# Kernel tuning notes

Hardware: AMD Instinct MI355X
Metric: run time of the kernel (lower is better)

The kernel has to match this reference:

```python
import jax, jax.numpy as jnp
import numpy as np

L, B = 64, 7          # n_layers, n_bit_options
EPS = 0.02            # sinkhorn entropic regularizer
ITERS = 200           # sinkhorn iterations
TINY = 1e-40


def setup_inputs() -> dict:
    key = jax.random.key(0)
    k1, k2, k3, k4 = jax.random.split(key, 4)
    theta = jax.random.normal(k1, (L, B), dtype=jnp.float32)
    phi = jax.random.normal(k2, (B,), dtype=jnp.float32)
    # layer sizes (param counts), positive; matches layer_sizes buffer usage
    n = jax.random.uniform(k3, (L,), dtype=jnp.float32, minval=4096.0, maxval=262144.0)
    sens = jax.random.uniform(k4, (L,), dtype=jnp.float32)
    sens = sens / sens.sum()  # update_sensitivity normalizes to a distribution
    bits = jnp.arange(2, 2 + B, dtype=jnp.float32)
    err = 2.0 ** (-2.0 * bits)  # quantization error per bitwidth
    return {"theta": theta, "phi": phi, "n": n, "sens": sens, "err": err}


def reference(theta, phi, n, sens, err):
    # DiffAllocator.compute_P
    a = n / n.sum()                         # row marginal (buffer 'a')
    b = jax.nn.softmax(phi)                 # col marginal b()
    C = (n * sens)[:, None] * err[None, :]  # build_cost: [L,B]
    K = -(C - theta) / EPS                  # log-kernel
    log_a = jnp.log(a + TINY)
    log_b = jnp.log(b + TINY)
    f0 = jnp.zeros((L,), dtype=theta.dtype)
    g0 = jnp.zeros((B,), dtype=theta.dtype)

    def step(carry, _):
        f, g = carry
        f = log_a - jax.scipy.special.logsumexp(K + g[None, :], axis=1)
        g = log_b - jax.scipy.special.logsumexp(K + f[:, None], axis=0)
        return (f, g), None

    (f, g), _ = jax.lax.scan(step, (f0, g0), None, length=ITERS)
    P = jnp.exp(K + f[:, None] + g[None, :])
    return P / (P.sum() + TINY)
```

## Files before the change

kernel.cpp:

```cpp
#include <hip/hip_runtime.h>
#include <math.h>

#define NB 7
#define EPS_ 0.02f
#define ITERS1_ 120
#define ITERS2_ 80
#define TINY_ 1e-40f
#define LOG2E_ 1.4426950408889634f
#define LN2_   0.6931471805599453f

__device__ __forceinline__ float exp2_hw(float x) {
#if __has_builtin(__builtin_amdgcn_exp2f)
    return __builtin_amdgcn_exp2f(x);
#else
    return __expf(x * LN2_);
#endif
}
__device__ __forceinline__ float log2_hw(float x) {
#if __has_builtin(__builtin_amdgcn_logf)
    return __builtin_amdgcn_logf(x);
#else
    return __logf(x) * LOG2E_;
#endif
}
__device__ __forceinline__ float rcp_hw(float x) {
#if __has_builtin(__builtin_amdgcn_rcpf)
    return __builtin_amdgcn_rcpf(x);
#else
    return 1.0f / x;
#endif
}

template <int CTRL>
__device__ __forceinline__ float dpp_ident(float identity, float x) {
    return __int_as_float(__builtin_amdgcn_update_dpp(
        __float_as_int(identity), __float_as_int(x), CTRL, 0xF, 0xF, false));
}
__device__ __forceinline__ float readlane63(float x) {
    return __int_as_float(__builtin_amdgcn_readlane(__float_as_int(x), 63));
}
__device__ __forceinline__ float wave_sum_bcast(float s) {
    s += dpp_ident<0x111>(0.f, s);
    s += dpp_ident<0x112>(0.f, s);
    s += dpp_ident<0x114>(0.f, s);
    s += dpp_ident<0x118>(0.f, s);
    s += dpp_ident<0x142>(0.f, s);
    s += dpp_ident<0x143>(0.f, s);
    return readlane63(s);
}

#define WAVE_MAX7(v0,v1,v2,v3,v4,v5,v6, m0,m1,m2,m3,m4,m5,m6)                 \
  {                                                                           \
    float r0,r1,r2,r3,r4,r5,r6;                                               \
    asm("v_mov_b32 %0, %14\n\t"                                               \
        "v_mov_b32 %1, %15\n\t"                                               \
        "v_mov_b32 %2, %16\n\t"                                               \
        "v_mov_b32 %3, %17\n\t"                                               \
        "v_mov_b32 %4, %18\n\t"                                               \
        "v_mov_b32 %5, %19\n\t"                                               \
        "v_mov_b32 %6, %20\n\t"                                               \
        "v_max_f32_dpp %0, %0, %0 row_shr:1 row_mask:0xf bank_mask:0xf\n\t"   \
        "v_max_f32_dpp %1, %1, %1 row_shr:1 row_mask:0xf bank_mask:0xf\n\t"   \
        "v_max_f32_dpp %2, %2, %2 row_shr:1 row_mask:0xf bank_mask:0xf\n\t"   \
        "v_max_f32_dpp %3, %3, %3 row_shr:1 row_mask:0xf bank_mask:0xf\n\t"   \
        "v_max_f32_dpp %4, %4, %4 row_shr:1 row_mask:0xf bank_mask:0xf\n\t"   \
        "v_max_f32_dpp %5, %5, %5 row_shr:1 row_mask:0xf bank_mask:0xf\n\t"   \
        "v_max_f32_dpp %6, %6, %6 row_shr:1 row_mask:0xf bank_mask:0xf\n\t"   \
        "v_max_f32_dpp %0, %0, %0 row_shr:2 row_mask:0xf bank_mask:0xf\n\t"   \
        "v_max_f32_dpp %1, %1, %1 row_shr:2 row_mask:0xf bank_mask:0xf\n\t"   \
        "v_max_f32_dpp %2, %2, %2 row_shr:2 row_mask:0xf bank_mask:0xf\n\t"   \
        "v_max_f32_dpp %3, %3, %3 row_shr:2 row_mask:0xf bank_mask:0xf\n\t"   \
        "v_max_f32_dpp %4, %4, %4 row_shr:2 row_mask:0xf bank_mask:0xf\n\t"   \
        "v_max_f32_dpp %5, %5, %5 row_shr:2 row_mask:0xf bank_mask:0xf\n\t"   \
        "v_max_f32_dpp %6, %6, %6 row_shr:2 row_mask:0xf bank_mask:0xf\n\t"   \
        "v_max_f32_dpp %0, %0, %0 row_shr:4 row_mask:0xf bank_mask:0xf\n\t"   \
        "v_max_f32_dpp %1, %1, %1 row_shr:4 row_mask:0xf bank_mask:0xf\n\t"   \
        "v_max_f32_dpp %2, %2, %2 row_shr:4 row_mask:0xf bank_mask:0xf\n\t"   \
        "v_max_f32_dpp %3, %3, %3 row_shr:4 row_mask:0xf bank_mask:0xf\n\t"   \
        "v_max_f32_dpp %4, %4, %4 row_shr:4 row_mask:0xf bank_mask:0xf\n\t"   \
        "v_max_f32_dpp %5, %5, %5 row_shr:4 row_mask:0xf bank_mask:0xf\n\t"   \
        "v_max_f32_dpp %6, %6, %6 row_shr:4 row_mask:0xf bank_mask:0xf\n\t"   \
        "v_max_f32_dpp %0, %0, %0 row_shr:8 row_mask:0xf bank_mask:0xf\n\t"   \
        "v_max_f32_dpp %1, %1, %1 row_shr:8 row_mask:0xf bank_mask:0xf\n\t"   \
        "v_max_f32_dpp %2, %2, %2 row_shr:8 row_mask:0xf bank_mask:0xf\n\t"   \
        "v_max_f32_dpp %3, %3, %3 row_shr:8 row_mask:0xf bank_mask:0xf\n\t"   \
        "v_max_f32_dpp %4, %4, %4 row_shr:8 row_mask:0xf bank_mask:0xf\n\t"   \
        "v_max_f32_dpp %5, %5, %5 row_shr:8 row_mask:0xf bank_mask:0xf\n\t"   \
        "v_max_f32_dpp %6, %6, %6 row_shr:8 row_mask:0xf bank_mask:0xf\n\t"   \
        "v_max_f32_dpp %0, %0, %0 row_bcast:15 row_mask:0xa bank_mask:0xf\n\t"\
        "v_max_f32_dpp %1, %1, %1 row_bcast:15 row_mask:0xa bank_mask:0xf\n\t"\
        "v_max_f32_dpp %2, %2, %2 row_bcast:15 row_mask:0xa bank_mask:0xf\n\t"\
        "v_max_f32_dpp %3, %3, %3 row_bcast:15 row_mask:0xa bank_mask:0xf\n\t"\
        "v_max_f32_dpp %4, %4, %4 row_bcast:15 row_mask:0xa bank_mask:0xf\n\t"\
        "v_max_f32_dpp %5, %5, %5 row_bcast:15 row_mask:0xa bank_mask:0xf\n\t"\
        "v_max_f32_dpp %6, %6, %6 row_bcast:15 row_mask:0xa bank_mask:0xf\n\t"\
        "v_max_f32_dpp %0, %0, %0 row_bcast:31 row_mask:0xc bank_mask:0xf\n\t"\
        "v_max_f32_dpp %1, %1, %1 row_bcast:31 row_mask:0xc bank_mask:0xf\n\t"\
        "v_max_f32_dpp %2, %2, %2 row_bcast:31 row_mask:0xc bank_mask:0xf\n\t"\
        "v_max_f32_dpp %3, %3, %3 row_bcast:31 row_mask:0xc bank_mask:0xf\n\t"\
        "v_max_f32_dpp %4, %4, %4 row_bcast:31 row_mask:0xc bank_mask:0xf\n\t"\
        "v_max_f32_dpp %5, %5, %5 row_bcast:31 row_mask:0xc bank_mask:0xf\n\t"\
        "v_max_f32_dpp %6, %6, %6 row_bcast:31 row_mask:0xc bank_mask:0xf\n\t"\
        "v_readlane_b32 %7, %0, 63\n\t"                                       \
        "v_readlane_b32 %8, %1, 63\n\t"                                       \
        "v_readlane_b32 %9, %2, 63\n\t"                                       \
        "v_readlane_b32 %10, %3, 63\n\t"                                      \
        "v_readlane_b32 %11, %4, 63\n\t"                                      \
        "v_readlane_b32 %12, %5, 63\n\t"                                      \
        "v_readlane_b32 %13, %6, 63\n\t"                                      \
        "s_nop 1"                                                             \
        : "=&v"(r0), "=&v"(r1), "=&v"(r2), "=&v"(r3),                         \
          "=&v"(r4), "=&v"(r5), "=&v"(r6),                                    \
          "=s"(m0), "=s"(m1), "=s"(m2), "=s"(m3),                             \
          "=s"(m4), "=s"(m5), "=s"(m6)                                        \
        : "v"(v0), "v"(v1), "v"(v2), "v"(v3), "v"(v4), "v"(v5), "v"(v6));     \
  }

#define WAVE_SUM7(e0,e1,e2,e3,e4,e5,e6, s0_,s1_,s2_,s3_,s4_,s5_,s6_)          \
    asm("s_nop 1\n\t"                                                         \
        "v_add_f32_dpp %0, %0, %0 row_shr:1 row_mask:0xf bank_mask:0xf\n\t"   \
        "v_add_f32_dpp %1, %1, %1 row_shr:1 row_mask:0xf bank_mask:0xf\n\t"   \
        "v_add_f32_dpp %2, %2, %2 row_shr:1 row_mask:0xf bank_mask:0xf\n\t"   \
        "v_add_f32_dpp %3, %3, %3 row_shr:1 row_mask:0xf bank_mask:0xf\n\t"   \
        "v_add_f32_dpp %4, %4, %4 row_shr:1 row_mask:0xf bank_mask:0xf\n\t"   \
        "v_add_f32_dpp %5, %5, %5 row_shr:1 row_mask:0xf bank_mask:0xf\n\t"   \
        "v_add_f32_dpp %6, %6, %6 row_shr:1 row_mask:0xf bank_mask:0xf\n\t"   \
        "v_add_f32_dpp %0, %0, %0 row_shr:2 row_mask:0xf bank_mask:0xf\n\t"   \
        "v_add_f32_dpp %1, %1, %1 row_shr:2 row_mask:0xf bank_mask:0xf\n\t"   \
        "v_add_f32_dpp %2, %2, %2 row_shr:2 row_mask:0xf bank_mask:0xf\n\t"   \
        "v_add_f32_dpp %3, %3, %3 row_shr:2 row_mask:0xf bank_mask:0xf\n\t"   \
        "v_add_f32_dpp %4, %4, %4 row_shr:2 row_mask:0xf bank_mask:0xf\n\t"   \
        "v_add_f32_dpp %5, %5, %5 row_shr:2 row_mask:0xf bank_mask:0xf\n\t"   \
        "v_add_f32_dpp %6, %6, %6 row_shr:2 row_mask:0xf bank_mask:0xf\n\t"   \
        "v_add_f32_dpp %0, %0, %0 row_shr:4 row_mask:0xf bank_mask:0xf\n\t"   \
        "v_add_f32_dpp %1, %1, %1 row_shr:4 row_mask:0xf bank_mask:0xf\n\t"   \
        "v_add_f32_dpp %2, %2, %2 row_shr:4 row_mask:0xf bank_mask:0xf\n\t"   \
        "v_add_f32_dpp %3, %3, %3 row_shr:4 row_mask:0xf bank_mask:0xf\n\t"   \
        "v_add_f32_dpp %4, %4, %4 row_shr:4 row_mask:0xf bank_mask:0xf\n\t"   \
        "v_add_f32_dpp %5, %5, %5 row_shr:4 row_mask:0xf bank_mask:0xf\n\t"   \
        "v_add_f32_dpp %6, %6, %6 row_shr:4 row_mask:0xf bank_mask:0xf\n\t"   \
        "v_add_f32_dpp %0, %0, %0 row_shr:8 row_mask:0xf bank_mask:0xf\n\t"   \
        "v_add_f32_dpp %1, %1, %1 row_shr:8 row_mask:0xf bank_mask:0xf\n\t"   \
        "v_add_f32_dpp %2, %2, %2 row_shr:8 row_mask:0xf bank_mask:0xf\n\t"   \
        "v_add_f32_dpp %3, %3, %3 row_shr:8 row_mask:0xf bank_mask:0xf\n\t"   \
        "v_add_f32_dpp %4, %4, %4 row_shr:8 row_mask:0xf bank_mask:0xf\n\t"   \
        "v_add_f32_dpp %5, %5, %5 row_shr:8 row_mask:0xf bank_mask:0xf\n\t"   \
        "v_add_f32_dpp %6, %6, %6 row_shr:8 row_mask:0xf bank_mask:0xf\n\t"   \
        "v_add_f32_dpp %0, %0, %0 row_bcast:15 row_mask:0xa bank_mask:0xf\n\t"\
        "v_add_f32_dpp %1, %1, %1 row_bcast:15 row_mask:0xa bank_mask:0xf\n\t"\
        "v_add_f32_dpp %2, %2, %2 row_bcast:15 row_mask:0xa bank_mask:0xf\n\t"\
        "v_add_f32_dpp %3, %3, %3 row_bcast:15 row_mask:0xa bank_mask:0xf\n\t"\
        "v_add_f32_dpp %4, %4, %4 row_bcast:15 row_mask:0xa bank_mask:0xf\n\t"\
        "v_add_f32_dpp %5, %5, %5 row_bcast:15 row_mask:0xa bank_mask:0xf\n\t"\
        "v_add_f32_dpp %6, %6, %6 row_bcast:15 row_mask:0xa bank_mask:0xf\n\t"\
        "v_add_f32_dpp %0, %0, %0 row_bcast:31 row_mask:0xc bank_mask:0xf\n\t"\
        "v_add_f32_dpp %1, %1, %1 row_bcast:31 row_mask:0xc bank_mask:0xf\n\t"\
        "v_add_f32_dpp %2, %2, %2 row_bcast:31 row_mask:0xc bank_mask:0xf\n\t"\
        "v_add_f32_dpp %3, %3, %3 row_bcast:31 row_mask:0xc bank_mask:0xf\n\t"\
        "v_add_f32_dpp %4, %4, %4 row_bcast:31 row_mask:0xc bank_mask:0xf\n\t"\
        "v_add_f32_dpp %5, %5, %5 row_bcast:31 row_mask:0xc bank_mask:0xf\n\t"\
        "v_add_f32_dpp %6, %6, %6 row_bcast:31 row_mask:0xc bank_mask:0xf\n\t"\
        "v_readlane_b32 %7, %0, 63\n\t"                                       \
        "v_readlane_b32 %8, %1, 63\n\t"                                       \
        "v_readlane_b32 %9, %2, 63\n\t"                                       \
        "v_readlane_b32 %10, %3, 63\n\t"                                      \
        "v_readlane_b32 %11, %4, 63\n\t"                                      \
        "v_readlane_b32 %12, %5, 63\n\t"                                      \
        "v_readlane_b32 %13, %6, 63\n\t"                                      \
        "s_nop 1"                                                             \
        : "+v"(e0), "+v"(e1), "+v"(e2), "+v"(e3),                             \
          "+v"(e4), "+v"(e5), "+v"(e6),                                       \
          "=s"(s0_), "=s"(s1_), "=s"(s2_), "=s"(s3_),                         \
          "=s"(s4_), "=s"(s5_), "=s"(s6_))

#define WAVE_SUM7_SRC(w0,w1,w2,w3,w4,w5,w6, s0_,s1_,s2_,s3_,s4_,s5_,s6_)     \
  {                                                                           \
    float r0,r1,r2,r3,r4,r5,r6;                                               \
    asm("s_nop 1\n\t"                                                         \
        "v_add_f32_dpp %0, %14, %14 row_shr:1 row_mask:0xf bank_mask:0xf\n\t" \
        "v_add_f32_dpp %1, %15, %15 row_shr:1 row_mask:0xf bank_mask:0xf\n\t" \
        "v_add_f32_dpp %2, %16, %16 row_shr:1 row_mask:0xf bank_mask:0xf\n\t" \
        "v_add_f32_dpp %3, %17, %17 row_shr:1 row_mask:0xf bank_mask:0xf\n\t" \
        "v_add_f32_dpp %4, %18, %18 row_shr:1 row_mask:0xf bank_mask:0xf\n\t" \
        "v_add_f32_dpp %5, %19, %19 row_shr:1 row_mask:0xf bank_mask:0xf\n\t" \
        "v_add_f32_dpp %6, %20, %20 row_shr:1 row_mask:0xf bank_mask:0xf\n\t" \
        "v_add_f32_dpp %0, %0, %0 row_shr:2 row_mask:0xf bank_mask:0xf\n\t"   \
        "v_add_f32_dpp %1, %1, %1 row_shr:2 row_mask:0xf bank_mask:0xf\n\t"   \
        "v_add_f32_dpp %2, %2, %2 row_shr:2 row_mask:0xf bank_mask:0xf\n\t"   \
        "v_add_f32_dpp %3, %3, %3 row_shr:2 row_mask:0xf bank_mask:0xf\n\t"   \
        "v_add_f32_dpp %4, %4, %4 row_shr:2 row_mask:0xf bank_mask:0xf\n\t"   \
        "v_add_f32_dpp %5, %5, %5 row_shr:2 row_mask:0xf bank_mask:0xf\n\t"   \
        "v_add_f32_dpp %6, %6, %6 row_shr:2 row_mask:0xf bank_mask:0xf\n\t"   \
        "v_add_f32_dpp %0, %0, %0 row_shr:4 row_mask:0xf bank_mask:0xf\n\t"   \
        "v_add_f32_dpp %1, %1, %1 row_shr:4 row_mask:0xf bank_mask:0xf\n\t"   \
        "v_add_f32_dpp %2, %2, %2 row_shr:4 row_mask:0xf bank_mask:0xf\n\t"   \
        "v_add_f32_dpp %3, %3, %3 row_shr:4 row_mask:0xf bank_mask:0xf\n\t"   \
        "v_add_f32_dpp %4, %4, %4 row_shr:4 row_mask:0xf bank_mask:0xf\n\t"   \
        "v_add_f32_dpp %5, %5, %5 row_shr:4 row_mask:0xf bank_mask:0xf\n\t"   \
        "v_add_f32_dpp %6, %6, %6 row_shr:4 row_mask:0xf bank_mask:0xf\n\t"   \
        "v_add_f32_dpp %0, %0, %0 row_shr:8 row_mask:0xf bank_mask:0xf\n\t"   \
        "v_add_f32_dpp %1, %1, %1 row_shr:8 row_mask:0xf bank_mask:0xf\n\t"   \
        "v_add_f32_dpp %2, %2, %2 row_shr:8 row_mask:0xf bank_mask:0xf\n\t"   \
        "v_add_f32_dpp %3, %3, %3 row_shr:8 row_mask:0xf bank_mask:0xf\n\t"   \
        "v_add_f32_dpp %4, %4, %4 row_shr:8 row_mask:0xf bank_mask:0xf\n\t"   \
        "v_add_f32_dpp %5, %5, %5 row_shr:8 row_mask:0xf bank_mask:0xf\n\t"   \
        "v_add_f32_dpp %6, %6, %6 row_shr:8 row_mask:0xf bank_mask:0xf\n\t"   \
        "v_add_f32_dpp %0, %0, %0 row_bcast:15 row_mask:0xa bank_mask:0xf\n\t"\
        "v_add_f32_dpp %1, %1, %1 row_bcast:15 row_mask:0xa bank_mask:0xf\n\t"\
        "v_add_f32_dpp %2, %2, %2 row_bcast:15 row_mask:0xa bank_mask:0xf\n\t"\
        "v_add_f32_dpp %3, %3, %3 row_bcast:15 row_mask:0xa bank_mask:0xf\n\t"\
        "v_add_f32_dpp %4, %4, %4 row_bcast:15 row_mask:0xa bank_mask:0xf\n\t"\
        "v_add_f32_dpp %5, %5, %5 row_bcast:15 row_mask:0xa bank_mask:0xf\n\t"\
        "v_add_f32_dpp %6, %6, %6 row_bcast:15 row_mask:0xa bank_mask:0xf\n\t"\
        "v_add_f32_dpp %0, %0, %0 row_bcast:31 row_mask:0xc bank_mask:0xf\n\t"\
        "v_add_f32_dpp %1, %1, %1 row_bcast:31 row_mask:0xc bank_mask:0xf\n\t"\
        "v_add_f32_dpp %2, %2, %2 row_bcast:31 row_mask:0xc bank_mask:0xf\n\t"\
        "v_add_f32_dpp %3, %3, %3 row_bcast:31 row_mask:0xc bank_mask:0xf\n\t"\
        "v_add_f32_dpp %4, %4, %4 row_bcast:31 row_mask:0xc bank_mask:0xf\n\t"\
        "v_add_f32_dpp %5, %5, %5 row_bcast:31 row_mask:0xc bank_mask:0xf\n\t"\
        "v_add_f32_dpp %6, %6, %6 row_bcast:31 row_mask:0xc bank_mask:0xf\n\t"\
        "v_readlane_b32 %7, %0, 63\n\t"                                       \
        "v_readlane_b32 %8, %1, 63\n\t"                                       \
        "v_readlane_b32 %9, %2, 63\n\t"                                       \
        "v_readlane_b32 %10, %3, 63\n\t"                                      \
        "v_readlane_b32 %11, %4, 63\n\t"                                      \
        "v_readlane_b32 %12, %5, 63\n\t"                                      \
        "v_readlane_b32 %13, %6, 63\n\t"                                      \
        "s_nop 1"                                                             \
        : "=&v"(r0), "=&v"(r1), "=&v"(r2), "=&v"(r3),                         \
          "=&v"(r4), "=&v"(r5), "=&v"(r6),                                    \
          "=s"(s0_), "=s"(s1_), "=s"(s2_), "=s"(s3_),                         \
          "=s"(s4_), "=s"(s5_), "=s"(s6_)                                     \
        : "v"(w0), "v"(w1), "v"(w2), "v"(w3), "v"(w4), "v"(w5), "v"(w6));     \
  }

__global__ __launch_bounds__(64) void sinkhorn_kernel(
    const float* __restrict__ theta,
    const float* __restrict__ phi,
    const float* __restrict__ n,
    const float* __restrict__ sens,
    const float* __restrict__ err,
    float* __restrict__ out)
{
    const int lane = threadIdx.x;

    const float ni = n[lane];
    const float si = sens[lane];

    const float kscale = LOG2E_ / EPS_;
    float K2[NB];
    #pragma unroll
    for (int j = 0; j < NB; ++j)
        K2[j] = (theta[lane * NB + j] - ni * si * err[j]) * kscale;

    const float nsum   = wave_sum_bcast(ni);
    const float aT     = ni / nsum + TINY_;
    const float log_a2 = log2_hw(aT);

    float t2v[NB];
    #pragma unroll
    for (int j = 0; j < NB; ++j) t2v[j] = phi[j] * LOG2E_;
    float pmax = t2v[0];
    #pragma unroll
    for (int j = 1; j < NB; ++j) pmax = fmaxf(pmax, t2v[j]);
    float psum = 0.f;
    #pragma unroll
    for (int j = 0; j < NB; ++j) psum += exp2_hw(t2v[j] - pmax);
    const float lps = log2_hw(psum);
    float bT[NB], log_b2[NB], cb[NB];
    #pragma unroll
    for (int j = 0; j < NB; ++j) {
        bT[j]     = exp2_hw(t2v[j] - pmax - lps) + TINY_;
        log_b2[j] = log2_hw(bT[j]);
        cb[j]     = log_b2[j] - log_a2;
    }

    float t[NB];
    #pragma unroll
    for (int j = 0; j < NB; ++j) t[j] = K2[j] - log_b2[j];

    const float LOF = __int_as_float(0x0D800000);
    const float HIF = __int_as_float(0x71800000);
    const unsigned LO = 0x0D800000u, HI = 0x71800000u;

    for (int it = 0; it < ITERS1_; ++it) {
        float a0 = t[0] + cb[0], a1 = t[1] + cb[1], a2 = t[2] + cb[2],
              a3 = t[3] + cb[3], a4 = t[4] + cb[4], a5 = t[5] + cb[5],
              a6 = t[6] + cb[6];
        float s = ((exp2_hw(a0) + exp2_hw(a1)) + (exp2_hw(a2) + exp2_hw(a3)))
                + ((exp2_hw(a4) + exp2_hw(a5)) + exp2_hw(a6));
        float L;
        const bool ok = (s >= LOF) && (s <= HIF);
        if (__ballot(ok) == ~0ull) {
            L = log2_hw(s);
        } else {
            float m = fmaxf(fmaxf(fmaxf(a0, a1), fmaxf(a2, a3)),
                            fmaxf(fmaxf(a4, a5), a6));
            float s2 = ((exp2_hw(a0 - m) + exp2_hw(a1 - m))
                      + (exp2_hw(a2 - m) + exp2_hw(a3 - m)))
                     + ((exp2_hw(a4 - m) + exp2_hw(a5 - m)) + exp2_hw(a6 - m));
            L = m + log2_hw(s2);
        }

        float q0 = t[0] - L, q1 = t[1] - L, q2 = t[2] - L, q3 = t[3] - L,
              q4 = t[4] - L, q5 = t[5] - L, q6 = t[6] - L;
        float e0 = exp2_hw(q0), e1 = exp2_hw(q1), e2 = exp2_hw(q2),
              e3 = exp2_hw(q3), e4 = exp2_hw(q4), e5 = exp2_hw(q5),
              e6 = exp2_hw(q6);
        float ss0, ss1, ss2, ss3, ss4, ss5, ss6;
        WAVE_SUM7(e0, e1, e2, e3, e4, e5, e6, ss0, ss1, ss2, ss3, ss4, ss5, ss6);

        const unsigned u0 = __float_as_uint(ss0), u1 = __float_as_uint(ss1),
                       u2 = __float_as_uint(ss2), u3 = __float_as_uint(ss3),
                       u4 = __float_as_uint(ss4), u5 = __float_as_uint(ss5),
                       u6 = __float_as_uint(ss6);
        const unsigned umin = min(min(min(u0, u1), min(u2, u3)),
                                  min(min(u4, u5), u6));
        const unsigned umax = max(max(max(u0, u1), max(u2, u3)),
                                  max(max(u4, u5), u6));
        if (umin < LO || umax > HI) {
            float M0, M1, M2, M3, M4, M5, M6;
            WAVE_MAX7(q0, q1, q2, q3, q4, q5, q6, M0, M1, M2, M3, M4, M5, M6);
            e0 = exp2_hw(q0 - M0); e1 = exp2_hw(q1 - M1);
            e2 = exp2_hw(q2 - M2); e3 = exp2_hw(q3 - M3);
            e4 = exp2_hw(q4 - M4); e5 = exp2_hw(q5 - M5);
            e6 = exp2_hw(q6 - M6);
            WAVE_SUM7(e0, e1, e2, e3, e4, e5, e6, ss0, ss1, ss2, ss3, ss4, ss5, ss6);
            t[0] = q0 - (M0 + log2_hw(ss0)); t[1] = q1 - (M1 + log2_hw(ss1));
            t[2] = q2 - (M2 + log2_hw(ss2)); t[3] = q3 - (M3 + log2_hw(ss3));
            t[4] = q4 - (M4 + log2_hw(ss4)); t[5] = q5 - (M5 + log2_hw(ss5));
            t[6] = q6 - (M6 + log2_hw(ss6));
        } else {
            t[0] = q0 - log2_hw(ss0); t[1] = q1 - log2_hw(ss1);
            t[2] = q2 - log2_hw(ss2); t[3] = q3 - log2_hw(ss3);
            t[4] = q4 - log2_hw(ss4); t[5] = q5 - log2_hw(ss5);
            t[6] = q6 - log2_hw(ss6);
        }
    }

    float U[NB], B[NB];
    #pragma unroll
    for (int j = 0; j < NB; ++j) {
        U[j] = exp2_hw(t[j]);
        B[j] = exp2_hw(cb[j]);
    }

    for (int it = 0; it < ITERS2_; ++it) {
        float p0 = U[0] * B[0], p1 = U[1] * B[1], p2 = U[2] * B[2],
              p3 = U[3] * B[3], p4 = U[4] * B[4], p5 = U[5] * B[5],
              p6 = U[6] * B[6];
        const float s = ((p0 + p1) + (p2 + p3)) + ((p4 + p5) + p6);
        const float rs = rcp_hw(s);
        float w0 = U[0] * rs, w1 = U[1] * rs, w2 = U[2] * rs,
              w3 = U[3] * rs, w4 = U[4] * rs, w5 = U[5] * rs,
              w6 = U[6] * rs;

        float ss0, ss1, ss2, ss3, ss4, ss5, ss6;
        WAVE_SUM7_SRC(w0, w1, w2, w3, w4, w5, w6,
                      ss0, ss1, ss2, ss3, ss4, ss5, ss6);

        const float r0 = rcp_hw(ss0);
        const float r1 = rcp_hw(ss1);
        const float r2 = rcp_hw(ss2);
        const float r3 = rcp_hw(ss3);
        const float r4 = rcp_hw(ss4);
        const float r5 = rcp_hw(ss5);
        const float r6 = rcp_hw(ss6);
        U[0] = w0 * r0; U[1] = w1 * r1; U[2] = w2 * r2; U[3] = w3 * r3;
        U[4] = w4 * r4; U[5] = w5 * r5; U[6] = w6 * r6;
    }

    float pr[NB];
    float rowsum = 0.f;
    #pragma unroll
    for (int j = 0; j < NB; ++j) {
        pr[j] = U[j] * bT[j];
        rowsum += pr[j];
    }
    const float total = wave_sum_bcast(rowsum);
    const float inv = 1.0f / (total + TINY_);
    #pragma unroll
    for (int j = 0; j < NB; ++j)
        out[lane * NB + j] = pr[j] * inv;
}

extern "C" void kernel_launch(void* const* d_in, const int* in_sizes, int n_in,
                              void* d_out, int out_size, void* d_ws, size_t ws_size,
                              hipStream_t stream) {
    const float* theta = (const float*)d_in[0];
    const float* phi   = (const float*)d_in[1];
    const float* n     = (const float*)d_in[2];
    const float* sens  = (const float*)d_in[3];
    const float* err   = (const float*)d_in[4];
    float* out = (float*)d_out;

    sinkhorn_kernel<<<1, 64, 0, stream>>>(theta, phi, n, sens, err, out);
}
```

Baseline: 115.2 us.

## Replace log-domain first Sinkhorn phase with mantissa/exponent scaled linear iteration

The first 120 Sinkhorn iterations no longer work in the log domain with exp2/log2 and data-dependent rescue branches. Each value is now kept as a mantissa plus an integer exponent. Rows are normalised with ldexp and a reciprocal, and columns are aligned with an integer wave-max over exponent offsets. This removes most transcendental instructions and the ballot-based fallback paths from the hot loop, at the cost of a wave integer-max reduction every iteration and a risk that precision handling differs from the reference.

```diff
diff --git a/kernel.cpp b/kernel.cpp
--- a/kernel.cpp
+++ b/kernel.cpp
@@ -28,6 +28,27 @@
     return __builtin_amdgcn_rcpf(x);
 #else
     return 1.0f / x;
+#endif
+}
+__device__ __forceinline__ float ldexp_hw(float x, int e) {
+#if __has_builtin(__builtin_amdgcn_ldexpf)
+    return __builtin_amdgcn_ldexpf(x, e);
+#else
+    float r; asm("v_ldexp_f32 %0, %1, %2" : "=v"(r) : "v"(x), "v"(e)); return r;
+#endif
+}
+__device__ __forceinline__ float frexp_mant_hw(float x) {
+#if __has_builtin(__builtin_amdgcn_frexp_mantf)
+    return __builtin_amdgcn_frexp_mantf(x);
+#else
+    float r; asm("v_frexp_mant_f32 %0, %1" : "=v"(r) : "v"(x)); return r;
+#endif
+}
+__device__ __forceinline__ int frexp_exp_hw(float x) {
+#if __has_builtin(__builtin_amdgcn_frexp_expf)
+    return __builtin_amdgcn_frexp_expf(x);
+#else
+    int r; asm("v_frexp_exp_i32_f32 %0, %1" : "=v"(r) : "v"(x)); return r;
 #endif
 }
 
@@ -49,58 +70,51 @@
     return readlane63(s);
 }
 
-#define WAVE_MAX7(v0,v1,v2,v3,v4,v5,v6, m0,m1,m2,m3,m4,m5,m6)                 \
+#define WAVE_MAXI7(v0,v1,v2,v3,v4,v5,v6, m0,m1,m2,m3,m4,m5,m6)               \
   {                                                                           \
-    float r0,r1,r2,r3,r4,r5,r6;                                               \
-    asm("v_mov_b32 %0, %14\n\t"                                               \
-        "v_mov_b32 %1, %15\n\t"                                               \
-        "v_mov_b32 %2, %16\n\t"                                               \
-        "v_mov_b32 %3, %17\n\t"                                               \
-        "v_mov_b32 %4, %18\n\t"                                               \
-        "v_mov_b32 %5, %19\n\t"                                               \
-        "v_mov_b32 %6, %20\n\t"                                               \
-        "v_max_f32_dpp %0, %0, %0 row_shr:1 row_mask:0xf bank_mask:0xf\n\t"   \
-        "v_max_f32_dpp %1, %1, %1 row_shr:1 row_mask:0xf bank_mask:0xf\n\t"   \
-        "v_max_f32_dpp %2, %2, %2 row_shr:1 row_mask:0xf bank_mask:0xf\n\t"   \
-        "v_max_f32_dpp %3, %3, %3 row_shr:1 row_mask:0xf bank_mask:0xf\n\t"   \
-        "v_max_f32_dpp %4, %4, %4 row_shr:1 row_mask:0xf bank_mask:0xf\n\t"   \
-        "v_max_f32_dpp %5, %5, %5 row_shr:1 row_mask:0xf bank_mask:0xf\n\t"   \
-        "v_max_f32_dpp %6, %6, %6 row_shr:1 row_mask:0xf bank_mask:0xf\n\t"   \
-        "v_max_f32_dpp %0, %0, %0 row_shr:2 row_mask:0xf bank_mask:0xf\n\t"   \
-        "v_max_f32_dpp %1, %1, %1 row_shr:2 row_mask:0xf bank_mask:0xf\n\t"   \
-        "v_max_f32_dpp %2, %2, %2 row_shr:2 row_mask:0xf bank_mask:0xf\n\t"   \
-        "v_max_f32_dpp %3, %3, %3 row_shr:2 row_mask:0xf bank_mask:0xf\n\t"   \
-        "v_max_f32_dpp %4, %4, %4 row_shr:2 row_mask:0xf bank_mask:0xf\n\t"   \
-        "v_max_f32_dpp %5, %5, %5 row_shr:2 row_mask:0xf bank_mask:0xf\n\t"   \
-        "v_max_f32_dpp %6, %6, %6 row_shr:2 row_mask:0xf bank_mask:0xf\n\t"   \
-        "v_max_f32_dpp %0, %0, %0 row_shr:4 row_mask:0xf bank_mask:0xf\n\t"   \
-        "v_max_f32_dpp %1, %1, %1 row_shr:4 row_mask:0xf bank_mask:0xf\n\t"   \
-        "v_max_f32_dpp %2, %2, %2 row_shr:4 row_mask:0xf bank_mask:0xf\n\t"   \
-        "v_max_f32_dpp %3, %3, %3 row_shr:4 row_mask:0xf bank_mask:0xf\n\t"   \
-        "v_max_f32_dpp %4, %4, %4 row_shr:4 row_mask:0xf bank_mask:0xf\n\t"   \
-        "v_max_f32_dpp %5, %5, %5 row_shr:4 row_mask:0xf bank_mask:0xf\n\t"   \
-        "v_max_f32_dpp %6, %6, %6 row_shr:4 row_mask:0xf bank_mask:0xf\n\t"   \
-        "v_max_f32_dpp %0, %0, %0 row_shr:8 row_mask:0xf bank_mask:0xf\n\t"   \
-        "v_max_f32_dpp %1, %1, %1 row_shr:8 row_mask:0xf bank_mask:0xf\n\t"   \
-        "v_max_f32_dpp %2, %2, %2 row_shr:8 row_mask:0xf bank_mask:0xf\n\t"   \
-        "v_max_f32_dpp %3, %3, %3 row_shr:8 row_mask:0xf bank_mask:0xf\n\t"   \
-        "v_max_f32_dpp %4, %4, %4 row_shr:8 row_mask:0xf bank_mask:0xf\n\t"   \
-        "v_max_f32_dpp %5, %5, %5 row_shr:8 row_mask:0xf bank_mask:0xf\n\t"   \
-        "v_max_f32_dpp %6, %6, %6 row_shr:8 row_mask:0xf bank_mask:0xf\n\t"   \
-        "v_max_f32_dpp %0, %0, %0 row_bcast:15 row_mask:0xa bank_mask:0xf\n\t"\
-        "v_max_f32_dpp %1, %1, %1 row_bcast:15 row_mask:0xa bank_mask:0xf\n\t"\
-        "v_max_f32_dpp %2, %2, %2 row_bcast:15 row_mask:0xa bank_mask:0xf\n\t"\
-        "v_max_f32_dpp %3, %3, %3 row_bcast:15 row_mask:0xa bank_mask:0xf\n\t"\
-        "v_max_f32_dpp %4, %4, %4 row_bcast:15 row_mask:0xa bank_mask:0xf\n\t"\
-        "v_max_f32_dpp %5, %5, %5 row_bcast:15 row_mask:0xa bank_mask:0xf\n\t"\
-        "v_max_f32_dpp %6, %6, %6 row_bcast:15 row_mask:0xa bank_mask:0xf\n\t"\
-        "v_max_f32_dpp %0, %0, %0 row_bcast:31 row_mask:0xc bank_mask:0xf\n\t"\
-        "v_max_f32_dpp %1, %1, %1 row_bcast:31 row_mask:0xc bank_mask:0xf\n\t"\
-        "v_max_f32_dpp %2, %2, %2 row_bcast:31 row_mask:0xc bank_mask:0xf\n\t"\
-        "v_max_f32_dpp %3, %3, %3 row_bcast:31 row_mask:0xc bank_mask:0xf\n\t"\
-        "v_max_f32_dpp %4, %4, %4 row_bcast:31 row_mask:0xc bank_mask:0xf\n\t"\
-        "v_max_f32_dpp %5, %5, %5 row_bcast:31 row_mask:0xc bank_mask:0xf\n\t"\
-        "v_max_f32_dpp %6, %6, %6 row_bcast:31 row_mask:0xc bank_mask:0xf\n\t"\
+    int r0,r1,r2,r3,r4,r5,r6;                                                 \
+    asm("v_max_i32_dpp %0, %14, %14 row_shr:1 row_mask:0xf bank_mask:0xf\n\t" \
+        "v_max_i32_dpp %1, %15, %15 row_shr:1 row_mask:0xf bank_mask:0xf\n\t" \
+        "v_max_i32_dpp %2, %16, %16 row_shr:1 row_mask:0xf bank_mask:0xf\n\t" \
+        "v_max_i32_dpp %3, %17, %17 row_shr:1 row_mask:0xf bank_mask:0xf\n\t" \
+        "v_max_i32_dpp %4, %18, %18 row_shr:1 row_mask:0xf bank_mask:0xf\n\t" \
+        "v_max_i32_dpp %5, %19, %19 row_shr:1 row_mask:0xf bank_mask:0xf\n\t" \
+        "v_max_i32_dpp %6, %20, %20 row_shr:1 row_mask:0xf bank_mask:0xf\n\t" \
+        "v_max_i32_dpp %0, %0, %0 row_shr:2 row_mask:0xf bank_mask:0xf\n\t"   \
+        "v_max_i32_dpp %1, %1, %1 row_shr:2 row_mask:0xf bank_mask:0xf\n\t"   \
+        "v_max_i32_dpp %2, %2, %2 row_shr:2 row_mask:0xf bank_mask:0xf\n\t"   \
+        "v_max_i32_dpp %3, %3, %3 row_shr:2 row_mask:0xf bank_mask:0xf\n\t"   \
+        "v_max_i32_dpp %4, %4, %4 row_shr:2 row_mask:0xf bank_mask:0xf\n\t"   \
+        "v_max_i32_dpp %5, %5, %5 row_shr:2 row_mask:0xf bank_mask:0xf\n\t"   \
+        "v_max_i32_dpp %6, %6, %6 row_shr:2 row_mask:0xf bank_mask:0xf\n\t"   \
+        "v_max_i32_dpp %0, %0, %0 row_shr:4 row_mask:0xf bank_mask:0xf\n\t"   \
+        "v_max_i32_dpp %1, %1, %1 row_shr:4 row_mask:0xf bank_mask:0xf\n\t"   \
+        "v_max_i32_dpp %2, %2, %2 row_shr:4 row_mask:0xf bank_mask:0xf\n\t"   \
+        "v_max_i32_dpp %3, %3, %3 row_shr:4 row_mask:0xf bank_mask:0xf\n\t"   \
+        "v_max_i32_dpp %4, %4, %4 row_shr:4 row_mask:0xf bank_mask:0xf\n\t"   \
+        "v_max_i32_dpp %5, %5, %5 row_shr:4 row_mask:0xf bank_mask:0xf\n\t"   \
+        "v_max_i32_dpp %6, %6, %6 row_shr:4 row_mask:0xf bank_mask:0xf\n\t"   \
+        "v_max_i32_dpp %0, %0, %0 row_shr:8 row_mask:0xf bank_mask:0xf\n\t"   \
+        "v_max_i32_dpp %1, %1, %1 row_shr:8 row_mask:0xf bank_mask:0xf\n\t"   \
+        "v_max_i32_dpp %2, %2, %2 row_shr:8 row_mask:0xf bank_mask:0xf\n\t"   \
+        "v_max_i32_dpp %3, %3, %3 row_shr:8 row_mask:0xf bank_mask:0xf\n\t"   \
+        "v_max_i32_dpp %4, %4, %4 row_shr:8 row_mask:0xf bank_mask:0xf\n\t"   \
+        "v_max_i32_dpp %5, %5, %5 row_shr:8 row_mask:0xf bank_mask:0xf\n\t"   \
+        "v_max_i32_dpp %6, %6, %6 row_shr:8 row_mask:0xf bank_mask:0xf\n\t"   \
+        "v_max_i32_dpp %0, %0, %0 row_bcast:15 row_mask:0xa bank_mask:0xf\n\t"\
+        "v_max_i32_dpp %1, %1, %1 row_bcast:15 row_mask:0xa bank_mask:0xf\n\t"\
+        "v_max_i32_dpp %2, %2, %2 row_bcast:15 row_mask:0xa bank_mask:0xf\n\t"\
+        "v_max_i32_dpp %3, %3, %3 row_bcast:15 row_mask:0xa bank_mask:0xf\n\t"\
+        "v_max_i32_dpp %4, %4, %4 row_bcast:15 row_mask:0xa bank_mask:0xf\n\t"\
+        "v_max_i32_dpp %5, %5, %5 row_bcast:15 row_mask:0xa bank_mask:0xf\n\t"\
+        "v_max_i32_dpp %6, %6, %6 row_bcast:15 row_mask:0xa bank_mask:0xf\n\t"\
+        "v_max_i32_dpp %0, %0, %0 row_bcast:31 row_mask:0xc bank_mask:0xf\n\t"\
+        "v_max_i32_dpp %1, %1, %1 row_bcast:31 row_mask:0xc bank_mask:0xf\n\t"\
+        "v_max_i32_dpp %2, %2, %2 row_bcast:31 row_mask:0xc bank_mask:0xf\n\t"\
+        "v_max_i32_dpp %3, %3, %3 row_bcast:31 row_mask:0xc bank_mask:0xf\n\t"\
+        "v_max_i32_dpp %4, %4, %4 row_bcast:31 row_mask:0xc bank_mask:0xf\n\t"\
+        "v_max_i32_dpp %5, %5, %5 row_bcast:31 row_mask:0xc bank_mask:0xf\n\t"\
+        "v_max_i32_dpp %6, %6, %6 row_bcast:31 row_mask:0xc bank_mask:0xf\n\t"\
         "v_readlane_b32 %7, %0, 63\n\t"                                       \
         "v_readlane_b32 %8, %1, 63\n\t"                                       \
         "v_readlane_b32 %9, %2, 63\n\t"                                       \
@@ -267,82 +281,81 @@
     #pragma unroll
     for (int j = 0; j < NB; ++j) psum += exp2_hw(t2v[j] - pmax);
     const float lps = log2_hw(psum);
-    float bT[NB], log_b2[NB], cb[NB];
+    float bT[NB], cb[NB];
     #pragma unroll
     for (int j = 0; j < NB; ++j) {
         bT[j]     = exp2_hw(t2v[j] - pmax - lps) + TINY_;
-        log_b2[j] = log2_hw(bT[j]);
-        cb[j]     = log_b2[j] - log_a2;
-    }
-
-    float t[NB];
-    #pragma unroll
-    for (int j = 0; j < NB; ++j) t[j] = K2[j] - log_b2[j];
-
-    const float LOF = __int_as_float(0x0D800000);
-    const float HIF = __int_as_float(0x71800000);
-    const unsigned LO = 0x0D800000u, HI = 0x71800000u;
+        const float log_b2 = log2_hw(bT[j]);
+        cb[j]     = log_b2 - log_a2;
+    }
+    float b2c[NB], ibc[NB];
+    #pragma unroll
+    for (int j = 0; j < NB; ++j) {
+        b2c[j] = exp2_hw(cb[j]);
+        ibc[j] = exp2_hw(-cb[j]);
+    }
+
+    float Mm[NB]; int iE[NB];
+    #pragma unroll
+    for (int j = 0; j < NB; ++j) {
+        const float y  = K2[j] - log_a2;
+        const float yi = rintf(y);
+        iE[j] = (int)yi;
+        Mm[j] = exp2_hw(y - yi);
+    }
 
     for (int it = 0; it < ITERS1_; ++it) {
-        float a0 = t[0] + cb[0], a1 = t[1] + cb[1], a2 = t[2] + cb[2],
-              a3 = t[3] + cb[3], a4 = t[4] + cb[4], a5 = t[5] + cb[5],
-              a6 = t[6] + cb[6];
-        float s = ((exp2_hw(a0) + exp2_hw(a1)) + (exp2_hw(a2) + exp2_hw(a3)))
-                + ((exp2_hw(a4) + exp2_hw(a5)) + exp2_hw(a6));
-        float L;
-        const bool ok = (s >= LOF) && (s <= HIF);
-        if (__ballot(ok) == ~0ull) {
-            L = log2_hw(s);
-        } else {
-            float m = fmaxf(fmaxf(fmaxf(a0, a1), fmaxf(a2, a3)),
-                            fmaxf(fmaxf(a4, a5), a6));
-            float s2 = ((exp2_hw(a0 - m) + exp2_hw(a1 - m))
-                      + (exp2_hw(a2 - m) + exp2_hw(a3 - m)))
-                     + ((exp2_hw(a4 - m) + exp2_hw(a5 - m)) + exp2_hw(a6 - m));
-            L = m + log2_hw(s2);
-        }
-
-        float q0 = t[0] - L, q1 = t[1] - L, q2 = t[2] - L, q3 = t[3] - L,
-              q4 = t[4] - L, q5 = t[5] - L, q6 = t[6] - L;
-        float e0 = exp2_hw(q0), e1 = exp2_hw(q1), e2 = exp2_hw(q2),
-              e3 = exp2_hw(q3), e4 = exp2_hw(q4), e5 = exp2_hw(q5),
-              e6 = exp2_hw(q6);
+        const int X = max(max(max(iE[0], iE[1]), max(iE[2], iE[3])),
+                          max(max(iE[4], iE[5]), iE[6]));
+        const int xe0 = iE[0]-X, xe1 = iE[1]-X, xe2 = iE[2]-X, xe3 = iE[3]-X,
+                  xe4 = iE[4]-X, xe5 = iE[5]-X, xe6 = iE[6]-X;
+        const float f0 = ldexp_hw(Mm[0], xe0), f1 = ldexp_hw(Mm[1], xe1),
+                    f2 = ldexp_hw(Mm[2], xe2), f3 = ldexp_hw(Mm[3], xe3),
+                    f4 = ldexp_hw(Mm[4], xe4), f5 = ldexp_hw(Mm[5], xe5),
+                    f6 = ldexp_hw(Mm[6], xe6);
+        const float s  = ((f0 + f1) + (f2 + f3)) + ((f4 + f5) + f6);
+        const float rs = rcp_hw(s);
+
+        int C0, C1, C2, C3, C4, C5, C6;
+        WAVE_MAXI7(xe0, xe1, xe2, xe3, xe4, xe5, xe6,
+                   C0, C1, C2, C3, C4, C5, C6);
+
+        const float g0 = (Mm[0]*ibc[0])*rs, g1 = (Mm[1]*ibc[1])*rs,
+                    g2 = (Mm[2]*ibc[2])*rs, g3 = (Mm[3]*ibc[3])*rs,
+                    g4 = (Mm[4]*ibc[4])*rs, g5 = (Mm[5]*ibc[5])*rs,
+                    g6 = (Mm[6]*ibc[6])*rs;
+        const int d0 = xe0-C0, d1 = xe1-C1, d2 = xe2-C2, d3 = xe3-C3,
+                  d4 = xe4-C4, d5 = xe5-C5, d6 = xe6-C6;
+        float h0 = ldexp_hw(g0, d0), h1 = ldexp_hw(g1, d1),
+              h2 = ldexp_hw(g2, d2), h3 = ldexp_hw(g3, d3),
+              h4 = ldexp_hw(g4, d4), h5 = ldexp_hw(g5, d5),
+              h6 = ldexp_hw(g6, d6);
+
         float ss0, ss1, ss2, ss3, ss4, ss5, ss6;
-        WAVE_SUM7(e0, e1, e2, e3, e4, e5, e6, ss0, ss1, ss2, ss3, ss4, ss5, ss6);
-
-        const unsigned u0 = __float_as_uint(ss0), u1 = __float_as_uint(ss1),
-                       u2 = __float_as_uint(ss2), u3 = __float_as_uint(ss3),
-                       u4 = __float_as_uint(ss4), u5 = __float_as_uint(ss5),
-                       u6 = __float_as_uint(ss6);
-        const unsigned umin = min(min(min(u0, u1), min(u2, u3)),
-                                  min(min(u4, u5), u6));
-        const unsigned umax = max(max(max(u0, u1), max(u2, u3)),
-                                  max(max(u4, u5), u6));
-        if (umin < LO || umax > HI) {
-            float M0, M1, M2, M3, M4, M5, M6;
-            WAVE_MAX7(q0, q1, q2, q3, q4, q5, q6, M0, M1, M2, M3, M4, M5, M6);
-            e0 = exp2_hw(q0 - M0); e1 = exp2_hw(q1 - M1);
-            e2 = exp2_hw(q2 - M2); e3 = exp2_hw(q3 - M3);
-            e4 = exp2_hw(q4 - M4); e5 = exp2_hw(q5 - M5);
-            e6 = exp2_hw(q6 - M6);
-            WAVE_SUM7(e0, e1, e2, e3, e4, e5, e6, ss0, ss1, ss2, ss3, ss4, ss5, ss6);
-            t[0] = q0 - (M0 + log2_hw(ss0)); t[1] = q1 - (M1 + log2_hw(ss1));
-            t[2] = q2 - (M2 + log2_hw(ss2)); t[3] = q3 - (M3 + log2_hw(ss3));
-            t[4] = q4 - (M4 + log2_hw(ss4)); t[5] = q5 - (M5 + log2_hw(ss5));
-            t[6] = q6 - (M6 + log2_hw(ss6));
-        } else {
-            t[0] = q0 - log2_hw(ss0); t[1] = q1 - log2_hw(ss1);
-            t[2] = q2 - log2_hw(ss2); t[3] = q3 - log2_hw(ss3);
-            t[4] = q4 - log2_hw(ss4); t[5] = q5 - log2_hw(ss5);
-            t[6] = q6 - log2_hw(ss6);
-        }
+        WAVE_SUM7(h0, h1, h2, h3, h4, h5, h6,
+                  ss0, ss1, ss2, ss3, ss4, ss5, ss6);
+
+        const float r0 = rcp_hw(ss0), r1 = rcp_hw(ss1), r2 = rcp_hw(ss2),
+                    r3 = rcp_hw(ss3), r4 = rcp_hw(ss4), r5 = rcp_hw(ss5),
+                    r6 = rcp_hw(ss6);
+        const float w0 = (g0*r0)*b2c[0], w1 = (g1*r1)*b2c[1],
+                    w2 = (g2*r2)*b2c[2], w3 = (g3*r3)*b2c[3],
+                    w4 = (g4*r4)*b2c[4], w5 = (g5*r5)*b2c[5],
+                    w6 = (g6*r6)*b2c[6];
+        Mm[0] = frexp_mant_hw(w0); iE[0] = frexp_exp_hw(w0) + d0;
+        Mm[1] = frexp_mant_hw(w1); iE[1] = frexp_exp_hw(w1) + d1;
+        Mm[2] = frexp_mant_hw(w2); iE[2] = frexp_exp_hw(w2) + d2;
+        Mm[3] = frexp_mant_hw(w3); iE[3] = frexp_exp_hw(w3) + d3;
+        Mm[4] = frexp_mant_hw(w4); iE[4] = frexp_exp_hw(w4) + d4;
+        Mm[5] = frexp_mant_hw(w5); iE[5] = frexp_exp_hw(w5) + d5;
+        Mm[6] = frexp_mant_hw(w6); iE[6] = frexp_exp_hw(w6) + d6;
     }
 
     float U[NB], B[NB];
     #pragma unroll
     for (int j = 0; j < NB; ++j) {
-        U[j] = exp2_hw(t[j]);
-        B[j] = exp2_hw(cb[j]);
+        U[j] = ldexp_hw(Mm[j] * ibc[j], iE[j]);
+        B[j] = b2c[j];
     }
 
     for (int it = 0; it < ITERS2_; ++it) {
```

Measured after the change: 120.3 us. 1.04x slower.
